# Optimization experiments

Measured on AMD Instinct MI355X. Metric: run time of the kernel, lower is better.

Reference implementation:

```python
import jax, jax.numpy as jnp
import numpy as np

# ---- config (from cfg / InstantNGP defaults) ----
W_IMG, H_IMG = 1024, 1024            # uv_reso_w, uv_reso_h
N_LEVELS = 16                        # standard InstantNGP level count
BASE_RES = 16
FINEST_RES = 1024                    # cfg['finest_level']
F_FEAT = 2                           # features per level
LOG2_T = 19                          # cfg['log2_hashmap_size']
T = 1 << LOG2_T
HIDDEN = 64
PRIMES = np.array([1, 2654435761], dtype=np.uint32)  # 2D spatial-hash primes


def setup_inputs() -> dict:
    key = jax.random.key(0)
    ks = jax.random.split(key, 5)
    d_in = N_LEVELS * F_FEAT
    tables = jax.random.uniform(ks[0], (N_LEVELS, T, F_FEAT), jnp.float32, -1e-4, 1e-4)
    W1 = jax.random.normal(ks[1], (d_in, HIDDEN), jnp.float32) / np.sqrt(d_in)
    b1 = jnp.zeros((HIDDEN,), jnp.float32)
    W2 = jax.random.normal(ks[2], (HIDDEN, HIDDEN), jnp.float32) / np.sqrt(HIDDEN)
    b2 = jnp.zeros((HIDDEN,), jnp.float32)
    W3 = jax.random.normal(ks[3], (HIDDEN, 3), jnp.float32) / np.sqrt(HIDDEN)
    b3 = jnp.zeros((3,), jnp.float32)
    return {"tables": tables, "W1": W1, "b1": b1, "W2": W2, "b2": b2, "W3": W3, "b3": b3}


def _uv_coords():
    # replicate torch.meshgrid(arange(W), arange(H), indexing='xy') -> (H, W)
    xx, yy = jnp.meshgrid(jnp.arange(W_IMG), jnp.arange(H_IMG), indexing='xy')
    x = xx.ravel().astype(jnp.float32) / W_IMG
    y = yy.ravel().astype(jnp.float32) / H_IMG
    return jnp.stack([x, y], axis=1)  # [N, 2]


def _hash_encode(coord, tables):
    # coord: [N,2] in [0,1); tables: [L,T,F]
    growth = np.exp((np.log(FINEST_RES) - np.log(BASE_RES)) / (N_LEVELS - 1))
    res = np.floor(BASE_RES * growth ** np.arange(N_LEVELS)).astype(np.float32)  # [L]
    scaled = coord[None, :, :] * res[:, None, None]          # [L,N,2]
    c0f = jnp.floor(scaled)
    frac = scaled - c0f                                       # [L,N,2]
    c0 = c0f.astype(jnp.uint32)
    corners = jnp.array([[0, 0], [1, 0], [0, 1], [1, 1]], dtype=jnp.uint32)  # [4,2]
    cc = c0[:, :, None, :] + corners[None, None]              # [L,N,4,2]
    idx = (cc[..., 0] * jnp.uint32(PRIMES[0])) ^ (cc[..., 1] * jnp.uint32(PRIMES[1]))
    idx = (idx & jnp.uint32(T - 1)).astype(jnp.int32)         # [L,N,4]
    feats = jax.vmap(lambda tab, i: tab[i])(tables, idx)      # [L,N,4,F] scattered gather
    cf = corners.astype(jnp.float32)                          # [4,2]
    # bilinear weights: prod over dims of (frac if corner bit else 1-frac)
    w = jnp.prod(cf[None, None] * frac[:, :, None, :] +
                 (1.0 - cf[None, None]) * (1.0 - frac[:, :, None, :]), axis=-1)  # [L,N,4]
    feat = jnp.einsum('lnc,lncf->lnf', w, feats)              # [L,N,F]
    return jnp.transpose(feat, (1, 0, 2)).reshape(-1, N_LEVELS * F_FEAT)  # [N, L*F]


def reference(tables, W1, b1, W2, b2, W3, b3):
    coord = _uv_coords()                                      # [N,2]
    enc = _hash_encode(coord, tables)                         # [N,32]
    h = jax.nn.relu(enc @ W1 + b1)
    h = jax.nn.relu(h @ W2 + b2)
    out = h @ W3 + b3                                         # [N,3]
    img = out.reshape(H_IMG, W_IMG, 3).transpose(2, 0, 1)     # [3,H,W]
    return jax.nn.sigmoid(img)[None, ...]                     # [1,3,H,W]
```

## Files before the change

kernel.cpp:

```cpp
#include <hip/hip_runtime.h>
#include <math.h>

#define NLEV   16
#define TSIZE  524288
#define TMASK  524287
#define NPIX   (1024*1024)

typedef __attribute__((ext_vector_type(8))) short s8v;
typedef __attribute__((ext_vector_type(4))) float f4v;

struct ResArr { float r[NLEV]; };
union Frag { unsigned int u[4]; s8v v; };

__device__ __forceinline__ unsigned short bf16_rn(float x) {
    unsigned int u = __builtin_bit_cast(unsigned int, x);
    u += 0x7fffu + ((u >> 16) & 1u);
    return (unsigned short)(u >> 16);
}
__device__ __forceinline__ unsigned int pk_bf16(float lo, float hi) {
    return __builtin_amdgcn_perm(__builtin_bit_cast(unsigned int, hi),
                                 __builtin_bit_cast(unsigned int, lo),
                                 0x07060302u);
}

__global__ __launch_bounds__(256) void prep_kernel(
    const float* __restrict__ W1, const float* __restrict__ W2,
    const float* __restrict__ W3, float* __restrict__ ws, ResArr res)
{
    const int t = threadIdx.x;
    if (t < NLEV) ws[t] = res.r[t];
    float* w3p = ws + 16;
    unsigned short* w1t = (unsigned short*)(ws + 272);
    unsigned short* w2t = w1t + 64 * 32;
    for (int i = t; i < 64 * 4; i += 256) {
        int r = i >> 2, c = i & 3;
        w3p[i] = (c < 3) ? W3[r * 3 + c] : 0.0f;
    }
    for (int i = t; i < 64 * 32; i += 256) {
        int n = i >> 5, k = i & 31;
        w1t[i] = bf16_rn(W1[k * 64 + n]);
    }
    for (int i = t; i < 64 * 64; i += 256) {
        int n = i >> 6, k = i & 63;
        w2t[i] = bf16_rn(W2[k * 64 + n]);
    }
}

__global__ __launch_bounds__(256, 4) void ngp_mfma_kernel(
    const float* __restrict__ tables,
    const float* __restrict__ b1, const float* __restrict__ b2,
    const float* __restrict__ b3,
    const float* __restrict__ ws, float* __restrict__ out)
{
    __shared__ unsigned int h1lds[4][2048];

    const int tid  = threadIdx.x;
    const int lane = tid & 63;
    const int wv   = tid >> 6;
    const int c15  = lane & 15;
    const int g    = lane >> 4;
    const int a7   = c15 & 7;
    const int xb   = blockIdx.x * 16;
    const int yb   = blockIdx.y * 16;

    const float4 rv = *(const float4*)(ws + g * 4);
    const float rr[4] = { rv.x, rv.y, rv.z, rv.w };
    const float xs = (float)(xb + c15) * (1.0f / 1024.0f);
    float yf[4];
    #pragma unroll
    for (int pt = 0; pt < 4; ++pt)
        yf[pt] = (float)(yb + wv * 4 + pt) * (1.0f / 1024.0f);

    const float2* __restrict__ tabg = (const float2*)tables + (size_t)(g * 4) * TSIZE;

    Frag bfrag[4];
    #pragma unroll
    for (int j = 0; j < 4; ++j) {
        const float r  = rr[j];
        const float sx = xs * r;
        const float fx0 = floorf(sx);
        const float fx  = sx - fx0;
        const unsigned int cx  = (unsigned int)fx0;
        const unsigned int cx1 = cx + 1u;
        const float2* __restrict__ tab = tabg + (size_t)j * TSIZE;
        float2 f[4][4];
        float fyv[4];
        #pragma unroll
        for (int pt = 0; pt < 4; ++pt) {
            const float sy  = yf[pt] * r;
            const float fy0 = floorf(sy);
            fyv[pt] = sy - fy0;
            const unsigned int cy  = (unsigned int)fy0;
            const unsigned int hy0 = cy * 2654435761u;
            const unsigned int hy1 = hy0 + 2654435761u;
            f[pt][0] = tab[(cx  ^ hy0) & TMASK];
            f[pt][1] = tab[(cx1 ^ hy0) & TMASK];
            f[pt][2] = tab[(cx  ^ hy1) & TMASK];
            f[pt][3] = tab[(cx1 ^ hy1) & TMASK];
        }
        #pragma unroll
        for (int pt = 0; pt < 4; ++pt) {
            const float fy  = fyv[pt];
            const float w00 = (1.0f - fx) * (1.0f - fy);
            const float w10 = fx          * (1.0f - fy);
            const float w01 = (1.0f - fx) * fy;
            const float w11 = fx          * fy;
            const float e0 = w00 * f[pt][0].x + w10 * f[pt][1].x
                           + w01 * f[pt][2].x + w11 * f[pt][3].x;
            const float e1 = w00 * f[pt][0].y + w10 * f[pt][1].y
                           + w01 * f[pt][2].y + w11 * f[pt][3].y;
            bfrag[pt].u[j] = pk_bf16(e0, e1);
        }
    }

    const unsigned short* __restrict__ w1t = (const unsigned short*)(ws + 272);
    const unsigned short* __restrict__ w2t = w1t + 64 * 32;
    Frag afr[4];
    #pragma unroll
    for (int mt = 0; mt < 4; ++mt)
        afr[mt].v = *(const s8v*)(w1t + (mt * 16 + c15) * 32 + g * 8);

    f4v acc1[4][4];
    #pragma unroll
    for (int mt = 0; mt < 4; ++mt)
        #pragma unroll
        for (int pt = 0; pt < 4; ++pt)
            acc1[mt][pt] = (f4v){0.f, 0.f, 0.f, 0.f};
    #pragma unroll
    for (int mt = 0; mt < 4; ++mt)
        #pragma unroll
        for (int pt = 0; pt < 4; ++pt)
            acc1[mt][pt] = __builtin_amdgcn_mfma_f32_16x16x32_bf16(
                afr[mt].v, bfrag[pt].v, acc1[mt][pt], 0, 0, 0);

    unsigned int* __restrict__ hw = &h1lds[wv][0];
    #pragma unroll
    for (int mt = 0; mt < 4; ++mt) {
        const float4 bb = *(const float4*)(b1 + mt * 16 + g * 4);
        #pragma unroll
        for (int pt = 0; pt < 4; ++pt) {
            const f4v v = acc1[mt][pt];
            const float v0 = fmaxf(v[0] + bb.x, 0.0f);
            const float v1 = fmaxf(v[1] + bb.y, 0.0f);
            const float v2 = fmaxf(v[2] + bb.z, 0.0f);
            const float v3 = fmaxf(v[3] + bb.w, 0.0f);
            unsigned int* dst = hw + ((pt * 16 + c15) << 5)
                                   + ((mt * 8 + g * 2) ^ (a7 << 2));
            dst[0] = pk_bf16(v0, v1);
            dst[1] = pk_bf16(v2, v3);
        }
    }

    f4v acc2[4][4];
    #pragma unroll
    for (int mt = 0; mt < 4; ++mt)
        #pragma unroll
        for (int pt = 0; pt < 4; ++pt)
            acc2[mt][pt] = (f4v){0.f, 0.f, 0.f, 0.f};
    #pragma unroll
    for (int st = 0; st < 2; ++st) {
        Frag a2[4], bf2[4];
        #pragma unroll
        for (int mt = 0; mt < 4; ++mt)
            a2[mt].v = *(const s8v*)(w2t + (mt * 16 + c15) * 64 + st * 32 + g * 8);
        #pragma unroll
        for (int pt = 0; pt < 4; ++pt)
            bf2[pt].v = *(const s8v*)(hw + ((pt * 16 + c15) << 5)
                                         + ((st * 16 + g * 4) ^ (a7 << 2)));
        #pragma unroll
        for (int mt = 0; mt < 4; ++mt)
            #pragma unroll
            for (int pt = 0; pt < 4; ++pt)
                acc2[mt][pt] = __builtin_amdgcn_mfma_f32_16x16x32_bf16(
                    a2[mt].v, bf2[pt].v, acc2[mt][pt], 0, 0, 0);
    }

    const float* __restrict__ w3p = ws + 16;
    float part[4][3] = {{0,0,0},{0,0,0},{0,0,0},{0,0,0}};
    #pragma unroll
    for (int mt = 0; mt < 4; ++mt) {
        const float4 bb2 = *(const float4*)(b2 + mt * 16 + g * 4);
        const float bbv[4] = { bb2.x, bb2.y, bb2.z, bb2.w };
        #pragma unroll
        for (int r = 0; r < 4; ++r) {
            const float4 w3 = *(const float4*)(w3p + (size_t)(mt * 16 + g * 4 + r) * 4);
            #pragma unroll
            for (int pt = 0; pt < 4; ++pt) {
                const float h = fmaxf(acc2[mt][pt][r] + bbv[r], 0.0f);
                part[pt][0] = fmaf(h, w3.x, part[pt][0]);
                part[pt][1] = fmaf(h, w3.y, part[pt][1]);
                part[pt][2] = fmaf(h, w3.z, part[pt][2]);
            }
        }
    }
    #pragma unroll
    for (int pt = 0; pt < 4; ++pt)
        #pragma unroll
        for (int c = 0; c < 3; ++c) {
            float v = part[pt][c];
            v += __shfl_xor(v, 16);
            v += __shfl_xor(v, 32);
            part[pt][c] = v;
        }
    float o0 = 0.f, o1 = 0.f, o2 = 0.f;
    #pragma unroll
    for (int pt = 0; pt < 4; ++pt) {
        if (g == pt) { o0 = part[pt][0]; o1 = part[pt][1]; o2 = part[pt][2]; }
    }
    o0 += b3[0]; o1 += b3[1]; o2 += b3[2];
    const int pix = ((yb + wv * 4 + g) << 10) + xb + c15;
    out[0 * NPIX + pix] = 1.0f / (1.0f + __expf(-o0));
    out[1 * NPIX + pix] = 1.0f / (1.0f + __expf(-o1));
    out[2 * NPIX + pix] = 1.0f / (1.0f + __expf(-o2));
}

extern "C" void kernel_launch(void* const* d_in, const int* in_sizes, int n_in,
                              void* d_out, int out_size, void* d_ws, size_t ws_size,
                              hipStream_t stream) {
    const float* tables = (const float*)d_in[0];
    const float* W1     = (const float*)d_in[1];
    const float* b1     = (const float*)d_in[2];
    const float* W2     = (const float*)d_in[3];
    const float* b2     = (const float*)d_in[4];
    const float* W3     = (const float*)d_in[5];
    const float* b3     = (const float*)d_in[6];
    float* out          = (float*)d_out;
    float* ws           = (float*)d_ws;

    ResArr res;
    const double growth = exp((log(1024.0) - log(16.0)) / 15.0);
    for (int l = 0; l < NLEV; ++l)
        res.r[l] = (float)floor(16.0 * pow(growth, (double)l));

    hipLaunchKernelGGL(prep_kernel, dim3(1), dim3(256), 0, stream, W1, W2, W3, ws, res);
    hipLaunchKernelGGL(ngp_mfma_kernel, dim3(64, 64), dim3(256), 0, stream,
                       tables, b1, b2, b3, ws, out);
}
```

Baseline: 71.87 us.

## Keep layer-1 activations in registers by permuting W2's K dimension

Removes the LDS round-trip between the first and second MFMA layers. The layer-1 accumulator layout is reused directly as the layer-2 B fragment, and the prepared W2 is permuted along K to match that register layout. This drops the shared-memory stores and loads and the 32KB LDS allocation, which could raise occupancy. It also fuses bias and ReLU per MFMA tile, which may change register pressure.

Result: slower. 75.32 us (+4.8%).

```diff
diff --git a/kernel.cpp b/kernel.cpp
--- a/kernel.cpp
+++ b/kernel.cpp
@@ -41,8 +41,9 @@
         w1t[i] = bf16_rn(W1[k * 64 + n]);
     }
     for (int i = t; i < 64 * 64; i += 256) {
-        int n = i >> 6, k = i & 63;
-        w2t[i] = bf16_rn(W2[k * 64 + n]);
+        int n2 = i >> 6, kp = i & 63;
+        int klog = (kp & 32) | ((kp & 4) << 2) | ((kp & 24) >> 1) | (kp & 3);
+        w2t[i] = bf16_rn(W2[klog * 64 + n2]);
     }
 }
 
@@ -52,14 +53,11 @@
     const float* __restrict__ b3,
     const float* __restrict__ ws, float* __restrict__ out)
 {
-    __shared__ unsigned int h1lds[4][2048];
-
     const int tid  = threadIdx.x;
     const int lane = tid & 63;
     const int wv   = tid >> 6;
     const int c15  = lane & 15;
     const int g    = lane >> 4;
-    const int a7   = c15 & 7;
     const int xb   = blockIdx.x * 16;
     const int yb   = blockIdx.y * 16;
 
@@ -115,39 +113,24 @@
 
     const unsigned short* __restrict__ w1t = (const unsigned short*)(ws + 272);
     const unsigned short* __restrict__ w2t = w1t + 64 * 32;
-    Frag afr[4];
-    #pragma unroll
-    for (int mt = 0; mt < 4; ++mt)
-        afr[mt].v = *(const s8v*)(w1t + (mt * 16 + c15) * 32 + g * 8);
-
-    f4v acc1[4][4];
-    #pragma unroll
-    for (int mt = 0; mt < 4; ++mt)
-        #pragma unroll
-        for (int pt = 0; pt < 4; ++pt)
-            acc1[mt][pt] = (f4v){0.f, 0.f, 0.f, 0.f};
-    #pragma unroll
-    for (int mt = 0; mt < 4; ++mt)
-        #pragma unroll
-        for (int pt = 0; pt < 4; ++pt)
-            acc1[mt][pt] = __builtin_amdgcn_mfma_f32_16x16x32_bf16(
-                afr[mt].v, bfrag[pt].v, acc1[mt][pt], 0, 0, 0);
-
-    unsigned int* __restrict__ hw = &h1lds[wv][0];
+
+    unsigned int hp[4][4][2];
     #pragma unroll
     for (int mt = 0; mt < 4; ++mt) {
+        Frag afr;
+        afr.v = *(const s8v*)(w1t + (mt * 16 + c15) * 32 + g * 8);
         const float4 bb = *(const float4*)(b1 + mt * 16 + g * 4);
         #pragma unroll
         for (int pt = 0; pt < 4; ++pt) {
-            const f4v v = acc1[mt][pt];
-            const float v0 = fmaxf(v[0] + bb.x, 0.0f);
-            const float v1 = fmaxf(v[1] + bb.y, 0.0f);
-            const float v2 = fmaxf(v[2] + bb.z, 0.0f);
-            const float v3 = fmaxf(v[3] + bb.w, 0.0f);
-            unsigned int* dst = hw + ((pt * 16 + c15) << 5)
-                                   + ((mt * 8 + g * 2) ^ (a7 << 2));
-            dst[0] = pk_bf16(v0, v1);
-            dst[1] = pk_bf16(v2, v3);
+            f4v acc = (f4v){0.f, 0.f, 0.f, 0.f};
+            acc = __builtin_amdgcn_mfma_f32_16x16x32_bf16(
+                afr.v, bfrag[pt].v, acc, 0, 0, 0);
+            const float v0 = fmaxf(acc[0] + bb.x, 0.0f);
+            const float v1 = fmaxf(acc[1] + bb.y, 0.0f);
+            const float v2 = fmaxf(acc[2] + bb.z, 0.0f);
+            const float v3 = fmaxf(acc[3] + bb.w, 0.0f);
+            hp[mt][pt][0] = pk_bf16(v0, v1);
+            hp[mt][pt][1] = pk_bf16(v2, v3);
         }
     }
 
@@ -164,9 +147,12 @@
         for (int mt = 0; mt < 4; ++mt)
             a2[mt].v = *(const s8v*)(w2t + (mt * 16 + c15) * 64 + st * 32 + g * 8);
         #pragma unroll
-        for (int pt = 0; pt < 4; ++pt)
-            bf2[pt].v = *(const s8v*)(hw + ((pt * 16 + c15) << 5)
-                                         + ((st * 16 + g * 4) ^ (a7 << 2)));
+        for (int pt = 0; pt < 4; ++pt) {
+            bf2[pt].u[0] = hp[2 * st + 0][pt][0];
+            bf2[pt].u[1] = hp[2 * st + 0][pt][1];
+            bf2[pt].u[2] = hp[2 * st + 1][pt][0];
+            bf2[pt].u[3] = hp[2 * st + 1][pt][1];
+        }
         #pragma unroll
         for (int mt = 0; mt < 4; ++mt)
             #pragma unroll
```
